# Kernel tuning notes

Measured on AMD Instinct MI355X. Metric: run time of the kernel, lower is better.

The kernel has to match this reference:

```python
import jax, jax.numpy as jnp
import numpy as np

B, S, E = 2, 2048, 1024
H = 16
DH = E // H
FF = 4096
LN_EPS = 1e-5


def setup_inputs() -> dict:
    key = jax.random.key(0)
    ks = jax.random.split(key, 8)
    s_in = 1.0 / np.sqrt(E)
    s_ff = 1.0 / np.sqrt(FF)
    return {
        "x": jax.random.normal(ks[0], (B, S, E), dtype=jnp.float32),
        "w_qkv": jax.random.normal(ks[1], (E, 3 * E), dtype=jnp.float32) * s_in,
        "b_qkv": jnp.zeros((3 * E,), dtype=jnp.float32),
        "w_proj": jax.random.normal(ks[2], (E, E), dtype=jnp.float32) * s_in,
        "b_proj": jnp.zeros((E,), dtype=jnp.float32),
        "ln_g": jnp.ones((E,), dtype=jnp.float32),
        "ln_b": jnp.zeros((E,), dtype=jnp.float32),
        "w1": jax.random.normal(ks[3], (E, FF), dtype=jnp.float32) * s_in,
        "b1": jnp.zeros((FF,), dtype=jnp.float32),
        "w2": jax.random.normal(ks[4], (FF, E), dtype=jnp.float32) * s_ff,
        "b2": jnp.zeros((E,), dtype=jnp.float32),
    }


def reference(x, w_qkv, b_qkv, w_proj, b_proj, ln_g, ln_b, w1, b1, w2, b2):
    b, s, e = x.shape
    scale = e ** 0.5  # NOTE: original scales by sqrt(embed_dim), not sqrt(head_dim)
    # qkv projection then raw view to [B,3,H,S,Dh] (faithful to torch .view)
    qkv = (x @ w_qkv + b_qkv).reshape(b, 3, H, s, DH)
    q, k, v = qkv[:, 0], qkv[:, 1], qkv[:, 2]  # each [B,H,S,Dh]
    scores = jnp.einsum("bhqd,bhkd->bhqk", q, k) / scale  # [B,H,S,S]
    causal = jnp.tril(jnp.ones((s, s), dtype=bool))
    scores = jnp.where(causal, scores, -jnp.inf)
    attn = jax.nn.softmax(scores, axis=-1)
    h = jnp.einsum("bhqk,bhkd->bhqd", attn, v)  # [B,H,S,Dh]
    h = h.reshape(b, s, e)  # faithful raw view back to [B,S,E]
    h = h @ w_proj + b_proj  # dropout = identity (eval)
    # add & norm
    h = h + x
    mu = jnp.mean(h, axis=-1, keepdims=True)
    var = jnp.var(h, axis=-1, keepdims=True)
    h = (h - mu) * jax.lax.rsqrt(var + LN_EPS) * ln_g + ln_b
    # FFN (dropouts = identity in eval)
    out = jax.nn.relu(h @ w1 + b1) @ w2 + b2
    return out
```

## Files before the change

kernel.cpp:

```cpp
#include <hip/hip_runtime.h>

#define B_ 2
#define S_ 2048
#define E_ 1024
#define H_ 16
#define DH_ 64
#define FF_ 4096

typedef unsigned short bf16_t;
typedef __attribute__((ext_vector_type(8))) short bfrag;
typedef __attribute__((ext_vector_type(4))) float f32x4;
typedef __attribute__((ext_vector_type(16))) float f32x16;
typedef __attribute__((ext_vector_type(4))) unsigned int u32x4;

__device__ __forceinline__ bf16_t f2bf(float x) {
  union { float f; unsigned u; } c; c.f = x;
  return (bf16_t)((c.u + 0x7fffu + ((c.u >> 16) & 1u)) >> 16);
}

__device__ __forceinline__ unsigned pkbf(float lo, float hi) {
  unsigned r;
  asm("v_cvt_pk_bf16_f32 %0, %1, %2" : "=v"(r) : "v"(lo), "v"(hi));
  return r;
}

__device__ __forceinline__ void gload16(const void* g, void* l) {
  __builtin_amdgcn_global_load_lds(
      (const __attribute__((address_space(1))) void*)g,
      (__attribute__((address_space(3))) void*)l, 16, 0, 0);
}

__global__ __launch_bounds__(256) void cvt_kernel(const float* __restrict__ s,
                                                  bf16_t* __restrict__ d) {
  const int i = blockIdx.x * 256 + threadIdx.x;
  const float4 v = ((const float4*)s)[i];
  union { bf16_t u[4]; uint2 uv; } o;
  o.u[0] = f2bf(v.x); o.u[1] = f2bf(v.y); o.u[2] = f2bf(v.z); o.u[3] = f2bf(v.w);
  *(uint2*)(d + (size_t)i * 4) = o.uv;
}

__global__ void transpose_cvt(const float* __restrict__ src, bf16_t* __restrict__ dst,
                              int R, int C) {
  __shared__ float tile[32][33];
  const int c0 = blockIdx.x * 32, r0 = blockIdx.y * 32;
  const int tx = threadIdx.x, ty = threadIdx.y;
#pragma unroll
  for (int i = 0; i < 32; i += 8)
    tile[ty + i][tx] = src[(size_t)(r0 + ty + i) * C + c0 + tx];
  __syncthreads();
#pragma unroll
  for (int i = 0; i < 32; i += 8)
    dst[(size_t)(c0 + ty + i) * R + r0 + tx] = f2bf(tile[tx][ty + i]);
}

__global__ void vtrans_kernel(const bf16_t* __restrict__ qkv, bf16_t* __restrict__ vt) {
  const int bh = blockIdx.z;
  const int b = bh >> 4, h = bh & 15;
  const bf16_t* src = qkv + (size_t)b * S_ * 3 * E_ + (size_t)2 * H_ * S_ * DH_ +
                      (size_t)h * S_ * DH_;
  bf16_t* dst = vt + (size_t)bh * DH_ * S_;
  const int s0 = blockIdx.x * 32, d0 = blockIdx.y * 32;
  __shared__ bf16_t tile[32][33];
  const int tx = threadIdx.x, ty = threadIdx.y;
#pragma unroll
  for (int i = 0; i < 32; i += 8)
    tile[ty + i][tx] = src[(size_t)(s0 + ty + i) * DH_ + d0 + tx];
  __syncthreads();
#pragma unroll
  for (int i = 0; i < 32; i += 8)
    dst[(size_t)(d0 + ty + i) * S_ + s0 + tx] = tile[tx][ty + i];
}


__device__ __forceinline__ void stage_half(const bf16_t* __restrict__ G, int row0,
                                           int kbyte, int Kbytes, bf16_t* ldsreg,
                                           int w, int l) {
#pragma unroll
  for (int j = 0; j < 2; ++j) {
    const int chunk = j * 8 + w;
    const int r = chunk * 8 + (l >> 3);
    const int slot = ((l & 7) ^ (r & 7)) << 4;
    const char* src = (const char*)G + (size_t)(row0 + r) * Kbytes + kbyte + slot;
    gload16(src, (char*)ldsreg + chunk * 1024);
  }
}

__device__ __forceinline__ bfrag ldfrag(const bf16_t* __restrict__ reg, int r, int ks,
                                        int l) {
  int cb = ks * 64 + ((l >> 4) << 4);
  cb ^= (r & 7) << 4;
  return *(const bfrag*)((const char*)reg + r * 128 + cb);
}

template <int MODE>
__global__ __launch_bounds__(512, 2) void gemm8(
    const bf16_t* __restrict__ A, const bf16_t* __restrict__ Bt,
    const float* __restrict__ bias, const float* __restrict__ resid,
    float* __restrict__ outF, bf16_t* __restrict__ outB,
    int M, int N, int K, int ktiles) {
  __shared__ __align__(16) bf16_t lds4[4][256 * 64];
  const int tid = threadIdx.x;
  const int w = tid >> 6, l = tid & 63;
  const int wr = (w >> 2) * 128, wc = (w & 3) * 64;
  const int m0t = blockIdx.y * 256, n0t = blockIdx.x * 256;
  const int Kb = K * 2;
  const int kt0 = (MODE == 4) ? (int)blockIdx.z * ktiles : 0;
  const int ktEnd = kt0 + ktiles;
  if (MODE == 4) outF += (size_t)blockIdx.z * (size_t)M * N;

  stage_half(A, m0t, kt0 * 128, Kb, lds4[0], w, l);
  stage_half(A, m0t + 128, kt0 * 128, Kb, lds4[0] + 8192, w, l);
  stage_half(Bt, n0t, kt0 * 128, Kb, lds4[1], w, l);
  stage_half(Bt, n0t + 128, kt0 * 128, Kb, lds4[1] + 8192, w, l);
  stage_half(Bt, n0t, (kt0 + 1) * 128, Kb, lds4[3], w, l);
  stage_half(Bt, n0t + 128, (kt0 + 1) * 128, Kb, lds4[3] + 8192, w, l);
  asm volatile("s_waitcnt vmcnt(4)" ::: "memory");
  __builtin_amdgcn_s_barrier();

  f32x4 acc[8][4] = {};
  const int fr = l & 15;

  for (int t2 = kt0; t2 < ktEnd; t2 += 2) {
#pragma unroll
    for (int d = 0; d < 2; ++d) {
      const bf16_t* Ar = lds4[d * 2];
      const bf16_t* Br = lds4[d * 2 + 1];
      int sa = t2 + 1 + d; if (sa >= ktEnd) sa = kt0;
      int sb = t2 + 2 + d; if (sb >= ktEnd) sb = kt0;
      bfrag bfr[4][2], afr[2][2];
#pragma unroll
      for (int p = 0; p < 4; ++p) {
        if (p == 0) {
#pragma unroll
          for (int n = 0; n < 4; ++n)
#pragma unroll
            for (int ks = 0; ks < 2; ++ks)
              bfr[n][ks] = ldfrag(Br, wc + n * 16 + fr, ks, l);
        }
#pragma unroll
        for (int mm = 0; mm < 2; ++mm)
#pragma unroll
          for (int ks = 0; ks < 2; ++ks)
            afr[mm][ks] = ldfrag(Ar, wr + p * 32 + mm * 16 + fr, ks, l);
        if (p == 0)      stage_half(A, m0t, sa * 128, Kb, lds4[(d ^ 1) * 2], w, l);
        else if (p == 1) stage_half(A, m0t + 128, sa * 128, Kb, lds4[(d ^ 1) * 2] + 8192, w, l);
        else if (p == 2) stage_half(Bt, n0t, sb * 128, Kb, lds4[d * 2 + 1], w, l);
        else             stage_half(Bt, n0t + 128, sb * 128, Kb, lds4[d * 2 + 1] + 8192, w, l);
        __builtin_amdgcn_s_barrier();
        asm volatile("s_waitcnt lgkmcnt(0)" ::: "memory");
        __builtin_amdgcn_sched_barrier(0);
        __builtin_amdgcn_s_setprio(1);
#pragma unroll
        for (int mm = 0; mm < 2; ++mm)
#pragma unroll
          for (int n = 0; n < 4; ++n)
#pragma unroll
            for (int ks = 0; ks < 2; ++ks)
              acc[p * 2 + mm][n] = __builtin_amdgcn_mfma_f32_16x16x32_bf16(
                  afr[mm][ks], bfr[n][ks], acc[p * 2 + mm][n], 0, 0, 0);
        __builtin_amdgcn_s_setprio(0);
        if (p == 3) asm volatile("s_waitcnt vmcnt(4)" ::: "memory");
        __builtin_amdgcn_s_barrier();
      }
    }
  }

  const int cr = (l >> 4) * 4, cc = l & 15;
#pragma unroll
  for (int n = 0; n < 4; ++n) {
    const int gc = n0t + wc + n * 16 + cc;
    const float bn = (MODE == 4) ? 0.f : bias[gc];
#pragma unroll
    for (int m = 0; m < 8; ++m) {
      const int gr0 = m0t + wr + m * 16 + cr;
#pragma unroll
      for (int j = 0; j < 4; ++j) {
        float v = acc[m][n][j] + bn;
        const size_t idx = (size_t)(gr0 + j) * N + gc;
        if (MODE == 1) v += resid[idx];
        if (MODE == 2) v = fmaxf(v, 0.f);
        if (MODE == 0 || MODE == 2) outB[idx] = f2bf(v);
        else outF[idx] = v;
      }
    }
  }
}

__global__ __launch_bounds__(256) void red4_kernel(const float* __restrict__ p,
                                                   const float* __restrict__ bias,
                                                   float* __restrict__ out) {
  const size_t i = ((size_t)blockIdx.x * 256 + threadIdx.x) * 4;
  const size_t PS = (size_t)4096 * 1024;
  const float4 a = *(const float4*)(p + i);
  const float4 b = *(const float4*)(p + PS + i);
  const float4 c = *(const float4*)(p + 2 * PS + i);
  const float4 d = *(const float4*)(p + 3 * PS + i);
  const float4 bb = *(const float4*)(bias + (i & 1023));
  float4 o;
  o.x = a.x + b.x + c.x + d.x + bb.x;
  o.y = a.y + b.y + c.y + d.y + bb.y;
  o.z = a.z + b.z + c.z + d.z + bb.z;
  o.w = a.w + b.w + c.w + d.w + bb.w;
  *(float4*)(out + i) = o;
}

#define C1_ 0.0450842213f

struct kf4 { bfrag k[4]; };

__device__ __forceinline__ kf4 loadK32(const bf16_t* __restrict__ Kp, int kv0,
                                       int lq32, int hi) {
  kf4 r;
#pragma unroll
  for (int c = 0; c < 4; ++c)
    r.k[c] = *(const bfrag*)&Kp[(size_t)(kv0 + lq32) * DH_ + c * 16 + hi * 8];
  return r;
}

template <bool MASK>
__device__ __forceinline__ void compute32(const kf4& s, const bf16_t* __restrict__ Vt,
                                          int kv0, const bfrag* qf, f32x16& o0,
                                          f32x16& o1, float& m, float& lsum,
                                          int lq32, int hi) {
  bfrag v00, v01, v10, v11;
  {
    const bf16_t* vr = &Vt[(size_t)lq32 * S_ + kv0 + hi * 8];
    v00 = *(const bfrag*)vr;
    v01 = *(const bfrag*)(vr + 16);
    const bf16_t* vr2 = &Vt[(size_t)(32 + lq32) * S_ + kv0 + hi * 8];
    v10 = *(const bfrag*)vr2;
    v11 = *(const bfrag*)(vr2 + 16);
  }
  f32x16 st;
#pragma unroll
  for (int j = 0; j < 16; ++j) st[j] = 0.f;
#pragma unroll
  for (int c = 0; c < 4; ++c)
    st = __builtin_amdgcn_mfma_f32_32x32x16_bf16(s.k[c], qf[c], st, 0, 0, 0);
  if (MASK) {
#pragma unroll
    for (int r = 0; r < 16; ++r) {
      const int kvloc = (r & 3) + 8 * (r >> 2) + 4 * hi;
      st[r] = (kvloc <= lq32) ? st[r] : -3.0e38f;
    }
  }
  float mx[8];
#pragma unroll
  for (int j = 0; j < 8; ++j) mx[j] = fmaxf(st[j], st[j + 8]);
#pragma unroll
  for (int stp = 4; stp >= 1; stp >>= 1)
#pragma unroll
    for (int j = 0; j < stp; ++j) mx[j] = fmaxf(mx[j], mx[j + stp]);
  float pm = fmaxf(mx[0], __shfl_xor(mx[0], 32));
  if (!__all(pm <= m + 128.0f)) {
    const float mn = fmaxf(m, pm);
    const float corr = exp2f((m - mn) * C1_);
    m = mn;
    lsum *= corr;
#pragma unroll
    for (int j = 0; j < 16; ++j) { o0[j] *= corr; o1[j] *= corr; }
  }
  const float mc = m * C1_;
  float p[16];
#pragma unroll
  for (int j = 0; j < 16; ++j) p[j] = exp2f(__builtin_fmaf(st[j], C1_, -mc));
  float sm[8];
#pragma unroll
  for (int j = 0; j < 8; ++j) sm[j] = p[j] + p[j + 8];
#pragma unroll
  for (int stp = 4; stp >= 1; stp >>= 1)
#pragma unroll
    for (int j = 0; j < stp; ++j) sm[j] += sm[j + stp];
  lsum += sm[0] + __shfl_xor(sm[0], 32);
  unsigned wv[8], ov[8];
#pragma unroll
  for (int j = 0; j < 8; ++j) wv[j] = pkbf(p[2 * j], p[2 * j + 1]);
#pragma unroll
  for (int j = 0; j < 8; ++j) ov[j] = (unsigned)__shfl_xor((int)wv[j], 32);
  union { unsigned u[4]; bfrag f; } f0, f1;
  f0.u[0] = hi ? ov[2] : wv[0];  f0.u[1] = hi ? ov[3] : wv[1];
  f0.u[2] = hi ? wv[2] : ov[0];  f0.u[3] = hi ? wv[3] : ov[1];
  f1.u[0] = hi ? ov[6] : wv[4];  f1.u[1] = hi ? ov[7] : wv[5];
  f1.u[2] = hi ? wv[6] : ov[4];  f1.u[3] = hi ? wv[7] : ov[5];
  o0 = __builtin_amdgcn_mfma_f32_32x32x16_bf16(v00, f0.f, o0, 0, 0, 0);
  o1 = __builtin_amdgcn_mfma_f32_32x32x16_bf16(v10, f0.f, o1, 0, 0, 0);
  o0 = __builtin_amdgcn_mfma_f32_32x32x16_bf16(v01, f1.f, o0, 0, 0, 0);
  o1 = __builtin_amdgcn_mfma_f32_32x32x16_bf16(v11, f1.f, o1, 0, 0, 0);
}

__global__ __launch_bounds__(256, 3) void attn_kernel(const bf16_t* __restrict__ qkv,
                                                      const bf16_t* __restrict__ vt,
                                                      bf16_t* __restrict__ outp) {
  __shared__ unsigned short ot[4][32 * 72];
  const int tid = threadIdx.x;
  const int w = tid >> 6, l = tid & 63;
  const int lq32 = l & 31, hi = l >> 5;
  const int by = blockIdx.y;
  const int b = by >> 4, h = by & 15;
  const int qt = (by & 16) ? (15 - (int)blockIdx.x) : (int)blockIdx.x;
  const size_t bbase = (size_t)b * S_ * 3 * E_;
  const bf16_t* Q = qkv + bbase + (size_t)h * S_ * DH_;
  const bf16_t* Kp = Q + (size_t)H_ * S_ * DH_;
  const bf16_t* Vt = vt + (size_t)by * DH_ * S_;
  bf16_t* Og = outp + (size_t)by * S_ * DH_;
  const int q0w = qt * 128 + w * 32;

  bfrag qf[4];
#pragma unroll
  for (int c = 0; c < 4; ++c)
    qf[c] = *(const bfrag*)&Q[(size_t)(q0w + lq32) * DH_ + c * 16 + hi * 8];

  f32x16 o0, o1;
#pragma unroll
  for (int j = 0; j < 16; ++j) { o0[j] = 0.f; o1[j] = 0.f; }
  float m = -3.0e38f, lsum = 0.f;

  const int nsteps = q0w >> 5;
  kf4 kcur = loadK32(Kp, 0, lq32, hi);
  for (int s = 0; s < nsteps; ++s) {
    kf4 knxt = loadK32(Kp, (s + 1) * 32, lq32, hi);
    compute32<false>(kcur, Vt, s * 32, qf, o0, o1, m, lsum, lq32, hi);
    kcur = knxt;
  }
  compute32<true>(kcur, Vt, q0w, qf, o0, o1, m, lsum, lq32, hi);

  const float linv = 1.0f / lsum;
  unsigned short* otw = ot[w];
#pragma unroll
  for (int t = 0; t < 2; ++t) {
    const f32x16& oo = t ? o1 : o0;
#pragma unroll
    for (int g = 0; g < 4; ++g) {
      const int d = t * 32 + g * 8 + hi * 4;
      uint2 v;
      v.x = pkbf(oo[g * 4 + 0] * linv, oo[g * 4 + 1] * linv);
      v.y = pkbf(oo[g * 4 + 2] * linv, oo[g * 4 + 3] * linv);
      *(uint2*)&otw[lq32 * 72 + d] = v;
    }
  }
  asm volatile("s_waitcnt lgkmcnt(0)" ::: "memory");
  const int q = l >> 1, hh = l & 1;
#pragma unroll
  for (int i = 0; i < 4; ++i) {
    u32x4 v = *(const u32x4*)&otw[q * 72 + hh * 32 + i * 8];
    *(u32x4*)&Og[(size_t)(q0w + q) * DH_ + hh * 32 + i * 8] = v;
  }
}

__device__ __forceinline__ void ln_core(float4 v, int t, const float* g,
                                        const float* be, bf16_t* orow) {
  float s = v.x + v.y + v.z + v.w;
  float q = v.x * v.x + v.y * v.y + v.z * v.z + v.w * v.w;
#pragma unroll
  for (int d = 1; d < 64; d <<= 1) { s += __shfl_xor(s, d); q += __shfl_xor(q, d); }
  __shared__ float red[8];
  const int w = t >> 6;
  if ((t & 63) == 0) { red[w] = s; red[4 + w] = q; }
  __syncthreads();
  s = red[0] + red[1] + red[2] + red[3];
  q = red[4] + red[5] + red[6] + red[7];
  const float mu = s * (1.f / E_);
  const float var = q * (1.f / E_) - mu * mu;
  const float rs = rsqrtf(var + 1e-5f);
  const float4 gg = ((const float4*)g)[t];
  const float4 bb = ((const float4*)be)[t];
  union { bf16_t u[4]; uint2 uv; } o;
  o.u[0] = f2bf((v.x - mu) * rs * gg.x + bb.x);
  o.u[1] = f2bf((v.y - mu) * rs * gg.y + bb.y);
  o.u[2] = f2bf((v.z - mu) * rs * gg.z + bb.z);
  o.u[3] = f2bf((v.w - mu) * rs * gg.w + bb.w);
  *(uint2*)(orow + t * 4) = o.uv;
}

__global__ __launch_bounds__(256) void ln_kernel(const float* __restrict__ hin,
                                                 const float* __restrict__ g,
                                                 const float* __restrict__ be,
                                                 bf16_t* __restrict__ outp) {
  const int row = blockIdx.x, t = threadIdx.x;
  const float4 v = ((const float4*)(hin + (size_t)row * E_))[t];
  ln_core(v, t, g, be, outp + (size_t)row * E_);
}

__global__ __launch_bounds__(256) void ln4_kernel(const float* __restrict__ p,
                                                  const float* __restrict__ x,
                                                  const float* __restrict__ bproj,
                                                  const float* __restrict__ g,
                                                  const float* __restrict__ be,
                                                  bf16_t* __restrict__ outp) {
  const int row = blockIdx.x, t = threadIdx.x;
  const size_t PS = (size_t)4096 * 1024;
  const size_t off = (size_t)row * E_ + t * 4;
  const float4 a = *(const float4*)(p + off);
  const float4 b = *(const float4*)(p + PS + off);
  const float4 c = *(const float4*)(p + 2 * PS + off);
  const float4 d = *(const float4*)(p + 3 * PS + off);
  const float4 xr = *(const float4*)(x + off);
  const float4 bp = *(const float4*)(bproj + t * 4);
  float4 v;
  v.x = a.x + b.x + c.x + d.x + xr.x + bp.x;
  v.y = a.y + b.y + c.y + d.y + xr.y + bp.y;
  v.z = a.z + b.z + c.z + d.z + xr.z + bp.z;
  v.w = a.w + b.w + c.w + d.w + xr.w + bp.w;
  ln_core(v, t, g, be, outp + (size_t)row * E_);
}

extern "C" void kernel_launch(void* const* d_in, const int* in_sizes, int n_in,
                              void* d_out, int out_size, void* d_ws, size_t ws_size,
                              hipStream_t stream) {
  (void)in_sizes; (void)n_in; (void)out_size;
  const float* x      = (const float*)d_in[0];
  const float* w_qkv  = (const float*)d_in[1];
  const float* b_qkv  = (const float*)d_in[2];
  const float* w_proj = (const float*)d_in[3];
  const float* b_proj = (const float*)d_in[4];
  const float* ln_g   = (const float*)d_in[5];
  const float* ln_b   = (const float*)d_in[6];
  const float* w1     = (const float*)d_in[7];
  const float* b1     = (const float*)d_in[8];
  const float* w2     = (const float*)d_in[9];
  const float* b2     = (const float*)d_in[10];
  float* out = (float*)d_out;
  char* ws = (char*)d_ws;
  const size_t MB = (size_t)1 << 20;
  bf16_t* w2T    = (bf16_t*)(ws + 0 * MB);
  bf16_t* w1T    = (bf16_t*)(ws + 8 * MB);
  bf16_t* vtb    = (bf16_t*)(ws + 16 * MB);
  bf16_t* lnb    = (bf16_t*)(ws + 16 * MB);
  bf16_t* wqkvT  = (bf16_t*)(ws + 24 * MB);
  bf16_t* wprojT = (bf16_t*)(ws + 30 * MB);
  bf16_t* attnb  = (bf16_t*)(ws + 32 * MB);
  bf16_t* xb     = (bf16_t*)(ws + 40 * MB);
  bf16_t* qkvb   = (bf16_t*)(ws + 48 * MB);
  float*  pparts = (float*)(ws + 48 * MB);
  bf16_t* ffn1s  = (bf16_t*)(ws + 80 * MB);
  float*  fparts = (float*)(ws + 16 * MB);
  float*  hbuf   = (float*)(ws + 48 * MB);
  bf16_t* ffn1f  = (bf16_t*)(ws + 48 * MB);
  const bool splitk = ws_size >= 112 * MB;

  dim3 tb(32, 8);
  cvt_kernel<<<4096, 256, 0, stream>>>(x, xb);
  transpose_cvt<<<dim3(3072 / 32, 1024 / 32), tb, 0, stream>>>(w_qkv, wqkvT, 1024, 3072);
  transpose_cvt<<<dim3(1024 / 32, 1024 / 32), tb, 0, stream>>>(w_proj, wprojT, 1024, 1024);
  transpose_cvt<<<dim3(4096 / 32, 1024 / 32), tb, 0, stream>>>(w1, w1T, 1024, 4096);
  transpose_cvt<<<dim3(1024 / 32, 4096 / 32), tb, 0, stream>>>(w2, w2T, 4096, 1024);

  gemm8<0><<<dim3(12, 16), 512, 0, stream>>>(xb, wqkvT, b_qkv, nullptr, nullptr, qkvb,
                                             4096, 3072, 1024, 16);

  vtrans_kernel<<<dim3(S_ / 32, 2, 32), tb, 0, stream>>>(qkvb, vtb);
  attn_kernel<<<dim3(16, 32), 256, 0, stream>>>(qkvb, vtb, attnb);

  if (splitk) {
    gemm8<4><<<dim3(4, 16, 4), 512, 0, stream>>>(attnb, wprojT, nullptr, nullptr,
                                                 pparts, nullptr, 4096, 1024, 1024, 4);
    ln4_kernel<<<4096, 256, 0, stream>>>(pparts, x, b_proj, ln_g, ln_b, lnb);
    gemm8<2><<<dim3(16, 16), 512, 0, stream>>>(lnb, w1T, b1, nullptr, nullptr, ffn1s,
                                               4096, 4096, 1024, 16);
    gemm8<4><<<dim3(4, 16, 4), 512, 0, stream>>>(ffn1s, w2T, nullptr, nullptr, fparts,
                                                 nullptr, 4096, 1024, 4096, 16);
    red4_kernel<<<4096, 256, 0, stream>>>(fparts, b2, out);
  } else {
    gemm8<1><<<dim3(4, 16), 512, 0, stream>>>(attnb, wprojT, b_proj, x, hbuf, nullptr,
                                              4096, 1024, 1024, 16);
    ln_kernel<<<4096, 256, 0, stream>>>(hbuf, ln_g, ln_b, lnb);
    gemm8<2><<<dim3(16, 16), 512, 0, stream>>>(lnb, w1T, b1, nullptr, nullptr, ffn1f,
                                               4096, 4096, 1024, 16);
    gemm8<3><<<dim3(4, 16), 512, 0, stream>>>(ffn1f, w2T, b2, nullptr, out, nullptr,
                                              4096, 1024, 4096, 64);
  }
}
```

Baseline: 248.7 us.

## Software-pipeline QK^T one step ahead of softmax and PV in attention

Restructures the attention inner loop so the QK^T MFMAs for the next KV tile are issued before the softmax and PV of the current tile. K is prefetched two tiles ahead, and V loads are split into a separate function. The MFMA sections are wrapped in s_setprio to favor matrix issue, and launch bounds drop from 3 to 2 waves per SIMD. The aim is to overlap matrix math with the exp/reduction work, at the cost of extra registers and lower occupancy.

Result: no change. 250.0 us (+0.5%).

```diff
diff --git a/kernel.cpp b/kernel.cpp
--- a/kernel.cpp
+++ b/kernel.cpp
@@ -207,6 +207,7 @@
 #define C1_ 0.0450842213f
 
 struct kf4 { bfrag k[4]; };
+struct vf4 { bfrag v[4]; };
 
 __device__ __forceinline__ kf4 loadK32(const bf16_t* __restrict__ Kp, int kv0,
                                        int lq32, int hi) {
@@ -217,26 +218,34 @@
   return r;
 }
 
-template <bool MASK>
-__device__ __forceinline__ void compute32(const kf4& s, const bf16_t* __restrict__ Vt,
-                                          int kv0, const bfrag* qf, f32x16& o0,
-                                          f32x16& o1, float& m, float& lsum,
-                                          int lq32, int hi) {
-  bfrag v00, v01, v10, v11;
-  {
-    const bf16_t* vr = &Vt[(size_t)lq32 * S_ + kv0 + hi * 8];
-    v00 = *(const bfrag*)vr;
-    v01 = *(const bfrag*)(vr + 16);
-    const bf16_t* vr2 = &Vt[(size_t)(32 + lq32) * S_ + kv0 + hi * 8];
-    v10 = *(const bfrag*)vr2;
-    v11 = *(const bfrag*)(vr2 + 16);
-  }
+__device__ __forceinline__ vf4 loadV32(const bf16_t* __restrict__ Vt, int kv0,
+                                       int lq32, int hi) {
+  vf4 r;
+  const bf16_t* vr = &Vt[(size_t)lq32 * S_ + kv0 + hi * 8];
+  r.v[0] = *(const bfrag*)vr;
+  r.v[1] = *(const bfrag*)(vr + 16);
+  const bf16_t* vr2 = &Vt[(size_t)(32 + lq32) * S_ + kv0 + hi * 8];
+  r.v[2] = *(const bfrag*)vr2;
+  r.v[3] = *(const bfrag*)(vr2 + 16);
+  return r;
+}
+
+__device__ __forceinline__ f32x16 qk32(const kf4& s, const bfrag* qf) {
   f32x16 st;
 #pragma unroll
   for (int j = 0; j < 16; ++j) st[j] = 0.f;
+  __builtin_amdgcn_s_setprio(1);
 #pragma unroll
   for (int c = 0; c < 4; ++c)
     st = __builtin_amdgcn_mfma_f32_32x32x16_bf16(s.k[c], qf[c], st, 0, 0, 0);
+  __builtin_amdgcn_s_setprio(0);
+  return st;
+}
+
+template <bool MASK>
+__device__ __forceinline__ void smpv(f32x16 st, const vf4& vv, f32x16& o0,
+                                     f32x16& o1, float& m, float& lsum, int lq32,
+                                     int hi) {
   if (MASK) {
 #pragma unroll
     for (int r = 0; r < 16; ++r) {
@@ -282,13 +291,15 @@
   f0.u[2] = hi ? wv[2] : ov[0];  f0.u[3] = hi ? wv[3] : ov[1];
   f1.u[0] = hi ? ov[6] : wv[4];  f1.u[1] = hi ? ov[7] : wv[5];
   f1.u[2] = hi ? wv[6] : ov[4];  f1.u[3] = hi ? wv[7] : ov[5];
-  o0 = __builtin_amdgcn_mfma_f32_32x32x16_bf16(v00, f0.f, o0, 0, 0, 0);
-  o1 = __builtin_amdgcn_mfma_f32_32x32x16_bf16(v10, f0.f, o1, 0, 0, 0);
-  o0 = __builtin_amdgcn_mfma_f32_32x32x16_bf16(v01, f1.f, o0, 0, 0, 0);
-  o1 = __builtin_amdgcn_mfma_f32_32x32x16_bf16(v11, f1.f, o1, 0, 0, 0);
-}
-
-__global__ __launch_bounds__(256, 3) void attn_kernel(const bf16_t* __restrict__ qkv,
+  __builtin_amdgcn_s_setprio(1);
+  o0 = __builtin_amdgcn_mfma_f32_32x32x16_bf16(vv.v[0], f0.f, o0, 0, 0, 0);
+  o1 = __builtin_amdgcn_mfma_f32_32x32x16_bf16(vv.v[2], f0.f, o1, 0, 0, 0);
+  o0 = __builtin_amdgcn_mfma_f32_32x32x16_bf16(vv.v[1], f1.f, o0, 0, 0, 0);
+  o1 = __builtin_amdgcn_mfma_f32_32x32x16_bf16(vv.v[3], f1.f, o1, 0, 0, 0);
+  __builtin_amdgcn_s_setprio(0);
+}
+
+__global__ __launch_bounds__(256, 2) void attn_kernel(const bf16_t* __restrict__ qkv,
                                                       const bf16_t* __restrict__ vt,
                                                       bf16_t* __restrict__ outp) {
   __shared__ unsigned short ot[4][32 * 72];
@@ -316,13 +327,20 @@
   float m = -3.0e38f, lsum = 0.f;
 
   const int nsteps = q0w >> 5;
-  kf4 kcur = loadK32(Kp, 0, lq32, hi);
+  kf4 kA = loadK32(Kp, 0, lq32, hi);
+  kf4 kB = loadK32(Kp, (nsteps ? 1 : 0) * 32, lq32, hi);
+  f32x16 stC = qk32(kA, qf);
   for (int s = 0; s < nsteps; ++s) {
-    kf4 knxt = loadK32(Kp, (s + 1) * 32, lq32, hi);
-    compute32<false>(kcur, Vt, s * 32, qf, o0, o1, m, lsum, lq32, hi);
-    kcur = knxt;
-  }
-  compute32<true>(kcur, Vt, q0w, qf, o0, o1, m, lsum, lq32, hi);
+    const int t2 = (s + 2 <= nsteps) ? (s + 2) : nsteps;
+    kf4 kN = loadK32(Kp, t2 * 32, lq32, hi);
+    vf4 vv = loadV32(Vt, s * 32, lq32, hi);
+    f32x16 stN = qk32(kB, qf);
+    smpv<false>(stC, vv, o0, o1, m, lsum, lq32, hi);
+    stC = stN;
+    kB = kN;
+  }
+  vf4 vv = loadV32(Vt, q0w, lq32, hi);
+  smpv<true>(stC, vv, o0, o1, m, lsum, lq32, hi);
 
   const float linv = 1.0f / lsum;
   unsigned short* otw = ot[w];
```

## Compute softmax row sums via MFMA with ones and merge weight transposes

Applied to the files above, without the earlier changes.

The attention kernel now accumulates the softmax denominator with extra MFMA ops that multiply a bf16 ones fragment by the probability fragments. This replaces the per-lane reduction tree and cross-lane shuffle. The sum is now taken from bf16-rounded probabilities and costs another 16-register accumulator, so launch bounds drop from 3 to 2 blocks per SM. Separately, the four weight transpose-convert launches are merged into one launch that picks its matrix by block index, removing launch overhead.

Result: faster. 243.2 us (-2.2%).

```diff
diff --git a/kernel.cpp b/kernel.cpp
--- a/kernel.cpp
+++ b/kernel.cpp
@@ -39,10 +39,19 @@
   *(uint2*)(d + (size_t)i * 4) = o.uv;
 }
 
-__global__ void transpose_cvt(const float* __restrict__ src, bf16_t* __restrict__ dst,
-                              int R, int C) {
+__global__ void transpose4_cvt(const float* __restrict__ s0, bf16_t* __restrict__ d0,
+                               const float* __restrict__ s1, bf16_t* __restrict__ d1,
+                               const float* __restrict__ s2, bf16_t* __restrict__ d2,
+                               const float* __restrict__ s3, bf16_t* __restrict__ d3) {
   __shared__ float tile[32][33];
-  const int c0 = blockIdx.x * 32, r0 = blockIdx.y * 32;
+  const int bid = blockIdx.x;
+  const float* src; bf16_t* dst; int R, C, lid;
+  if (bid < 3072)      { src = s0; dst = d0; R = 1024; C = 3072; lid = bid; }
+  else if (bid < 4096) { src = s1; dst = d1; R = 1024; C = 1024; lid = bid - 3072; }
+  else if (bid < 8192) { src = s2; dst = d2; R = 1024; C = 4096; lid = bid - 4096; }
+  else                 { src = s3; dst = d3; R = 4096; C = 1024; lid = bid - 8192; }
+  const int ncx = C >> 5;
+  const int c0 = (lid % ncx) * 32, r0 = (lid / ncx) * 32;
   const int tx = threadIdx.x, ty = threadIdx.y;
 #pragma unroll
   for (int i = 0; i < 32; i += 8)
@@ -220,8 +229,12 @@
 template <bool MASK>
 __device__ __forceinline__ void compute32(const kf4& s, const bf16_t* __restrict__ Vt,
                                           int kv0, const bfrag* qf, f32x16& o0,
-                                          f32x16& o1, float& m, float& lsum,
+                                          f32x16& o1, f32x16& lacc, float& m,
                                           int lq32, int hi) {
+  const short onebf = (short)0x3F80;
+  bfrag ones;
+#pragma unroll
+  for (int j = 0; j < 8; ++j) ones[j] = onebf;
   bfrag v00, v01, v10, v11;
   {
     const bf16_t* vr = &Vt[(size_t)lq32 * S_ + kv0 + hi * 8];
@@ -256,22 +269,13 @@
     const float mn = fmaxf(m, pm);
     const float corr = exp2f((m - mn) * C1_);
     m = mn;
-    lsum *= corr;
-#pragma unroll
-    for (int j = 0; j < 16; ++j) { o0[j] *= corr; o1[j] *= corr; }
+#pragma unroll
+    for (int j = 0; j < 16; ++j) { o0[j] *= corr; o1[j] *= corr; lacc[j] *= corr; }
   }
   const float mc = m * C1_;
   float p[16];
 #pragma unroll
   for (int j = 0; j < 16; ++j) p[j] = exp2f(__builtin_fmaf(st[j], C1_, -mc));
-  float sm[8];
-#pragma unroll
-  for (int j = 0; j < 8; ++j) sm[j] = p[j] + p[j + 8];
-#pragma unroll
-  for (int stp = 4; stp >= 1; stp >>= 1)
-#pragma unroll
-    for (int j = 0; j < stp; ++j) sm[j] += sm[j + stp];
-  lsum += sm[0] + __shfl_xor(sm[0], 32);
   unsigned wv[8], ov[8];
 #pragma unroll
   for (int j = 0; j < 8; ++j) wv[j] = pkbf(p[2 * j], p[2 * j + 1]);
@@ -284,11 +288,13 @@
   f1.u[2] = hi ? wv[6] : ov[4];  f1.u[3] = hi ? wv[7] : ov[5];
   o0 = __builtin_amdgcn_mfma_f32_32x32x16_bf16(v00, f0.f, o0, 0, 0, 0);
   o1 = __builtin_amdgcn_mfma_f32_32x32x16_bf16(v10, f0.f, o1, 0, 0, 0);
+  lacc = __builtin_amdgcn_mfma_f32_32x32x16_bf16(ones, f0.f, lacc, 0, 0, 0);
   o0 = __builtin_amdgcn_mfma_f32_32x32x16_bf16(v01, f1.f, o0, 0, 0, 0);
   o1 = __builtin_amdgcn_mfma_f32_32x32x16_bf16(v11, f1.f, o1, 0, 0, 0);
-}
-
-__global__ __launch_bounds__(256, 3) void attn_kernel(const bf16_t* __restrict__ qkv,
+  lacc = __builtin_amdgcn_mfma_f32_32x32x16_bf16(ones, f1.f, lacc, 0, 0, 0);
+}
+
+__global__ __launch_bounds__(256, 2) void attn_kernel(const bf16_t* __restrict__ qkv,
                                                       const bf16_t* __restrict__ vt,
                                                       bf16_t* __restrict__ outp) {
   __shared__ unsigned short ot[4][32 * 72];
@@ -310,21 +316,21 @@
   for (int c = 0; c < 4; ++c)
     qf[c] = *(const bfrag*)&Q[(size_t)(q0w + lq32) * DH_ + c * 16 + hi * 8];
 
-  f32x16 o0, o1;
-#pragma unroll
-  for (int j = 0; j < 16; ++j) { o0[j] = 0.f; o1[j] = 0.f; }
-  float m = -3.0e38f, lsum = 0.f;
+  f32x16 o0, o1, lacc;
+#pragma unroll
+  for (int j = 0; j < 16; ++j) { o0[j] = 0.f; o1[j] = 0.f; lacc[j] = 0.f; }
+  float m = -3.0e38f;
 
   const int nsteps = q0w >> 5;
   kf4 kcur = loadK32(Kp, 0, lq32, hi);
   for (int s = 0; s < nsteps; ++s) {
     kf4 knxt = loadK32(Kp, (s + 1) * 32, lq32, hi);
-    compute32<false>(kcur, Vt, s * 32, qf, o0, o1, m, lsum, lq32, hi);
+    compute32<false>(kcur, Vt, s * 32, qf, o0, o1, lacc, m, lq32, hi);
     kcur = knxt;
   }
-  compute32<true>(kcur, Vt, q0w, qf, o0, o1, m, lsum, lq32, hi);
-
-  const float linv = 1.0f / lsum;
+  compute32<true>(kcur, Vt, q0w, qf, o0, o1, lacc, m, lq32, hi);
+
+  const float linv = 1.0f / lacc[0];
   unsigned short* otw = ot[w];
 #pragma unroll
   for (int t = 0; t < 2; ++t) {
@@ -440,10 +446,8 @@
 
   dim3 tb(32, 8);
   cvt_kernel<<<4096, 256, 0, stream>>>(x, xb);
-  transpose_cvt<<<dim3(3072 / 32, 1024 / 32), tb, 0, stream>>>(w_qkv, wqkvT, 1024, 3072);
-  transpose_cvt<<<dim3(1024 / 32, 1024 / 32), tb, 0, stream>>>(w_proj, wprojT, 1024, 1024);
-  transpose_cvt<<<dim3(4096 / 32, 1024 / 32), tb, 0, stream>>>(w1, w1T, 1024, 4096);
-  transpose_cvt<<<dim3(1024 / 32, 4096 / 32), tb, 0, stream>>>(w2, w2T, 4096, 1024);
+  transpose4_cvt<<<12288, tb, 0, stream>>>(w_qkv, wqkvT, w_proj, wprojT, w1, w1T,
+                                           w2, w2T);
 
   gemm8<0><<<dim3(12, 16), 512, 0, stream>>>(xb, wqkvT, b_qkv, nullptr, nullptr, qkvb,
                                              4096, 3072, 1024, 16);
```
